# Kernel tuning notes

Measured on AMD Instinct MI355X. Metric: run time of the kernel, lower is better.

The kernel has to match this reference:

```python
import jax, jax.numpy as jnp
import numpy as np

IN_F, OUT_F, GROUP, BITS = 4096, 11008, 128, 4
PACK = 32 // BITS            # 8 nibbles per int32 word
N_GROUPS = IN_F // GROUP     # 32
MASK = (1 << BITS) - 1       # 0xF
TOKENS = 2048


def setup_inputs() -> dict:
    key = jax.random.key(0)
    ks = jax.random.split(key, 6)
    x = jax.random.normal(ks[0], (TOKENS, IN_F), dtype=jnp.float32)
    qweight = jax.random.randint(ks[1], (IN_F // PACK, OUT_F), 0, 2147483647, dtype=jnp.int32)
    qzeros = jax.random.randint(ks[2], (N_GROUPS, OUT_F // PACK), 0, 2147483647, dtype=jnp.int32)
    qscales = jax.random.randint(ks[3], (N_GROUPS, OUT_F), 0, 256, dtype=jnp.int32)  # uint8 values
    qscales_zeros = jax.random.uniform(ks[4], (1, OUT_F), dtype=jnp.float32)
    qscales_scales = jax.random.uniform(ks[5], (1, OUT_F), dtype=jnp.float32) * 0.01
    g_idx = jnp.arange(IN_F, dtype=jnp.int32) // GROUP
    return dict(x=x, qweight=qweight, qzeros=qzeros, qscales=qscales,
                qscales_zeros=qscales_zeros, qscales_scales=qscales_scales, g_idx=g_idx)


def _dequantize(qweight, qzeros, qscales, qscales_zeros, qscales_scales, g_idx, dtype):
    shifts = jnp.arange(0, 32, BITS, dtype=jnp.int32)  # [8]
    # unpack weights: [in/8, 8, out] -> [in, out]
    w = (qweight[:, None, :] >> shifts[None, :, None]) & MASK
    w = w.reshape(-1, qweight.shape[-1])
    # unpack zero-points (+1 per original code): [n_groups, out/8, 8] -> [n_groups, out]
    z = (((qzeros[:, :, None] >> shifts[None, None, :]) & MASK) + 1)
    z = z.reshape(-1, qweight.shape[-1])
    # dequantize the uint8-quantized scales, then apply group-wise
    scales = (qscales.astype(dtype) - qscales_zeros) * qscales_scales  # [n_groups, out]
    return (w - z[g_idx]).astype(dtype) * scales[g_idx]                # [in, out]


def reference(x, qweight, qzeros, qscales, qscales_zeros, qscales_scales, g_idx):
    weight = _dequantize(qweight, qzeros, qscales, qscales_zeros, qscales_scales,
                         g_idx, x.dtype)
    return x @ weight  # bias disabled (disable_bias=True)
```

## Files before the change

kernel.cpp:

```cpp
#include <hip/hip_runtime.h>
#include <hip/hip_fp16.h>
#include <stdint.h>

#define IN_F   4096
#define OUT_F  11008
#define TOKENS 2048
#define BM 128
#define BN 128
#define BK2 128
#define NT2 (IN_F / BK2)
#define NGROUP 32
#define OPW (OUT_F / 8)

typedef _Float16 f16;
typedef __attribute__((ext_vector_type(2))) _Float16 f16x2;
typedef __attribute__((ext_vector_type(8))) _Float16 f16x8;
typedef __attribute__((ext_vector_type(4))) float f32x4;
typedef __attribute__((ext_vector_type(4))) int   i32x4;

typedef __attribute__((address_space(3))) uint32_t lds_u32_t;
typedef const __attribute__((address_space(1))) uint32_t glb_u32_t;

#define SB0() __builtin_amdgcn_sched_barrier(0)

static __device__ __forceinline__ void gload_lds16(const void* g, void* l) {
    __builtin_amdgcn_global_load_lds((glb_u32_t*)g, (lds_u32_t*)l, 16, 0, 0);
}

__global__ __launch_bounds__(256) void quant_x_kernel(const float* __restrict__ x,
                                                      char* __restrict__ xi,
                                                      float* __restrict__ aws) {
    __shared__ float red[4];
    const int row = blockIdx.x;
    const int tid = threadIdx.x;
    const float* xr = x + (size_t)row * IN_F + tid * 16;
    float v[16];
    #pragma unroll
    for (int p = 0; p < 4; ++p) {
        const float4 t = *reinterpret_cast<const float4*>(xr + p * 4);
        v[p * 4 + 0] = t.x; v[p * 4 + 1] = t.y; v[p * 4 + 2] = t.z; v[p * 4 + 3] = t.w;
    }
    float m = 0.f;
    #pragma unroll
    for (int p = 0; p < 16; ++p) m = fmaxf(m, fabsf(v[p]));
    #pragma unroll
    for (int off = 32; off > 0; off >>= 1) m = fmaxf(m, __shfl_xor(m, off));
    if ((tid & 63) == 0) red[tid >> 6] = m;
    __syncthreads();
    m = fmaxf(fmaxf(red[0], red[1]), fmaxf(red[2], red[3]));
    const float a   = m * (1.0f / 127.0f);
    const float inv = (m > 0.f) ? 127.0f / m : 0.f;
    if (tid == 0) aws[row] = a;
    const float MAGIC = 12582912.0f;
    uint32_t b[16];
    #pragma unroll
    for (int p = 0; p < 16; ++p)
        b[p] = __builtin_bit_cast(uint32_t, fmaf(v[p], inv, MAGIC)) & 0xFFu;
    i32x4 d;
    d[0] = (int)(b[0] | (b[2] << 8) | (b[4]  << 16) | (b[6]  << 24));
    d[1] = (int)(b[1] | (b[3] << 8) | (b[5]  << 16) | (b[7]  << 24));
    d[2] = (int)(b[8] | (b[10] << 8) | (b[12] << 16) | (b[14] << 24));
    d[3] = (int)(b[9] | (b[11] << 8) | (b[13] << 16) | (b[15] << 24));
    *reinterpret_cast<i32x4*>(xi + (size_t)row * IN_F + tid * 16) = d;
}

__global__ __launch_bounds__(512, 2) void qgemm_i8_kernel(
    const char*     __restrict__ xi,
    const float*    __restrict__ aws,
    const uint32_t* __restrict__ qweight,
    const uint32_t* __restrict__ qzeros,
    const int*      __restrict__ qscales,
    const float*    __restrict__ qscales_zeros,
    const float*    __restrict__ qscales_scales,
    float*          __restrict__ out)
{
    __shared__ __align__(16) char Ash[2][BM * BK2];
    __shared__ __align__(16) char Bsh[2][BN * BK2];

    const int tid  = threadIdx.x;
    const int lane = tid & 63;
    const int wid  = tid >> 6;
    const int wm   = wid >> 2;
    const int wn   = wid & 3;

    const int mt = blockIdx.x & 15;
    const int nt = blockIdx.x >> 4;
    const int m0 = mt * BM;
    const int n0 = nt * BN;

    const int colb = tid & 127;
    const int h    = tid >> 7;
    const int ncol = n0 + colb;
    const int boff0 = colb * BK2 + ((h)     ^ (colb & 7)) * 16;
    const int boff1 = colb * BK2 + ((h + 4) ^ (colb & 7)) * 16;
    const uint32_t* bptr = qweight + (size_t)(2 * h) * OUT_F + ncol;

    const int arow0 = tid >> 3, aslot0 = tid & 7;
    const int arow1 = (tid + 512) >> 3, aslot1 = (tid + 512) & 7;
    const char* asrc0 = xi + (size_t)(m0 + arow0) * IN_F + (aslot0 ^ (arow0 & 7)) * 16;
    const char* asrc1 = xi + (size_t)(m0 + arow1) * IN_F + (aslot1 ^ (arow1 & 7)) * 16;
    const int adst0 = tid * 16, adst1 = (tid + 512) * 16;

    const int lr = lane & 15;
    const int lo = lane >> 4;
    int aoffr[2][4], boffr[2][2], cread[2];
    #pragma unroll
    for (int ks = 0; ks < 2; ++ks) {
        #pragma unroll
        for (int f = 0; f < 4; ++f) {
            const int ra = wm * 64 + f * 16 + lr;
            aoffr[ks][f] = ra * BK2 + ((ks * 4 + lo) ^ (ra & 7)) * 16;
        }
        #pragma unroll
        for (int j = 0; j < 2; ++j) {
            const int rb = wn * 32 + j * 16 + lr;
            boffr[ks][j] = rb * BK2 + ((ks * 4 + lo) ^ (rb & 7)) * 16;
        }
    }
    cread[0] = n0 + wn * 32 + lr;
    cread[1] = cread[0] + 16;
    float qszr[2], qssr[2];
    #pragma unroll
    for (int j = 0; j < 2; ++j) {
        qszr[j] = qscales_zeros[cread[j]];
        qssr[j] = qscales_scales[cread[j]];
    }

    f32x4 acc[4][2];
    #pragma unroll
    for (int i = 0; i < 4; ++i)
        #pragma unroll
        for (int j = 0; j < 2; ++j) {
            f32x4 z = {0.f, 0.f, 0.f, 0.f};
            acc[i][j] = z;
        }

    auto load_bw = [&](int t_, uint32_t* w) {
        const uint32_t* p = bptr + (size_t)t_ * 16 * OUT_F;
        w[0] = p[0];
        w[1] = p[OUT_F];
        w[2] = p[(size_t)8 * OUT_F];
        w[3] = p[(size_t)9 * OUT_F];
    };
    auto mk_kz = [&](uint32_t zw_) -> uint32_t {
        const uint32_t znib = (zw_ >> ((ncol & 7) * 4)) & 0xFu;
        return (127u - znib) * 0x01010101u;
    };
    auto unpack16 = [&](uint32_t wa, uint32_t wb, uint32_t kz) -> i32x4 {
        i32x4 d;
        d[0] = (int)(((( wa      ) & 0x0F0F0F0Fu) + kz) ^ 0x80808080u);
        d[1] = (int)((((wa >> 4)  & 0x0F0F0F0Fu) + kz) ^ 0x80808080u);
        d[2] = (int)(((( wb      ) & 0x0F0F0F0Fu) + kz) ^ 0x80808080u);
        d[3] = (int)((((wb >> 4)  & 0x0F0F0F0Fu) + kz) ^ 0x80808080u);
        return d;
    };
    auto stage_B = [&](int buf, const uint32_t* w, uint32_t kz) {
        *reinterpret_cast<i32x4*>(&Bsh[buf][boff0]) = unpack16(w[0], w[1], kz);
        *reinterpret_cast<i32x4*>(&Bsh[buf][boff1]) = unpack16(w[2], w[3], kz);
    };
    auto stage_A = [&](int buf, int t_) {
        gload_lds16(asrc0 + (size_t)t_ * BK2, &Ash[buf][adst0]);
        gload_lds16(asrc1 + (size_t)t_ * BK2, &Ash[buf][adst1]);
    };
    auto compute = [&](int buf, const float* sc) {
        i32x4 D[4][2];
        {
            i32x4 af[4], bf[2];
            #pragma unroll
            for (int f = 0; f < 4; ++f)
                af[f] = *reinterpret_cast<const i32x4*>(&Ash[buf][aoffr[0][f]]);
            #pragma unroll
            for (int j = 0; j < 2; ++j)
                bf[j] = *reinterpret_cast<const i32x4*>(&Bsh[buf][boffr[0][j]]);
            __builtin_amdgcn_s_setprio(1);
            #pragma unroll
            for (int i = 0; i < 4; ++i)
                #pragma unroll
                for (int j = 0; j < 2; ++j) {
                    i32x4 z0 = {0, 0, 0, 0};
                    D[i][j] = __builtin_amdgcn_mfma_i32_16x16x64_i8(af[i], bf[j], z0, 0, 0, 0);
                }
            __builtin_amdgcn_s_setprio(0);
        }
        {
            i32x4 af[4], bf[2];
            #pragma unroll
            for (int f = 0; f < 4; ++f)
                af[f] = *reinterpret_cast<const i32x4*>(&Ash[buf][aoffr[1][f]]);
            #pragma unroll
            for (int j = 0; j < 2; ++j)
                bf[j] = *reinterpret_cast<const i32x4*>(&Bsh[buf][boffr[1][j]]);
            __builtin_amdgcn_s_setprio(1);
            #pragma unroll
            for (int i = 0; i < 4; ++i)
                #pragma unroll
                for (int j = 0; j < 2; ++j)
                    D[i][j] = __builtin_amdgcn_mfma_i32_16x16x64_i8(af[i], bf[j], D[i][j], 0, 0, 0);
            __builtin_amdgcn_s_setprio(0);
        }
        #pragma unroll
        for (int i = 0; i < 4; ++i)
            #pragma unroll
            for (int j = 0; j < 2; ++j) {
                acc[i][j].x += sc[j] * (float)D[i][j][0];
                acc[i][j].y += sc[j] * (float)D[i][j][1];
                acc[i][j].z += sc[j] * (float)D[i][j][2];
                acc[i][j].w += sc[j] * (float)D[i][j][3];
            }
    };

    uint32_t wE[4], wO[4];
    uint32_t zwE, zwO;
    int sfE[2], sfO[2];

    {
        uint32_t w0[4];
        load_bw(0, w0);
        const uint32_t kz0 = mk_kz(qzeros[ncol >> 3]);
        stage_A(0, 0);
        stage_B(0, w0, kz0);
        load_bw(1, wE);
        zwE = qzeros[OPW + (ncol >> 3)];
        #pragma unroll
        for (int j = 0; j < 2; ++j) sfE[j] = qscales[cread[j]];
        asm volatile("s_waitcnt vmcnt(0)" ::: "memory");
        asm volatile("s_waitcnt lgkmcnt(0)" ::: "memory");
        __builtin_amdgcn_s_barrier();
    }

#define BODY(C, T, WC, ZC, SFC, WL, ZL, SFL)                                      \
  {                                                                               \
    const int tn1_ = ((T) + 1 < NT2) ? (T) + 1 : NT2 - 1;                         \
    const int tn2_ = ((T) + 2 < NT2) ? (T) + 2 : NT2 - 1;                         \
    float scur_[2];                                                               \
    _Pragma("unroll") for (int j = 0; j < 2; ++j)                                 \
      scur_[j] = ((float)SFC[j] - qszr[j]) * qssr[j];                             \
    const uint32_t kz_ = mk_kz(ZC);                                               \
    stage_B((C) ^ 1, WC, kz_);                                                    \
    SB0();                                                                        \
    stage_A((C) ^ 1, tn1_);                                                       \
    SB0();                                                                        \
    load_bw(tn2_, WL);                                                            \
    ZL = qzeros[(size_t)tn2_ * OPW + (ncol >> 3)];                                \
    _Pragma("unroll") for (int j = 0; j < 2; ++j)                                 \
      SFL[j] = qscales[(size_t)tn1_ * OUT_F + cread[j]];                          \
    SB0();                                                                        \
    compute(C, scur_);                                                            \
    asm volatile("s_waitcnt vmcnt(7)" ::: "memory");                              \
    asm volatile("s_waitcnt lgkmcnt(0)" ::: "memory");                            \
    __builtin_amdgcn_s_barrier();                                                 \
  }

    for (int t = 0; t < NT2; t += 2) {
        BODY(0, t,     wE, zwE, sfE, wO, zwO, sfO)
        BODY(1, t + 1, wO, zwO, sfO, wE, zwE, sfE)
    }
#undef BODY

    const int orow = m0 + wm * 64 + lo * 4;
    const int ocol = n0 + wn * 32 + lr;
    #pragma unroll
    for (int i = 0; i < 4; ++i)
        #pragma unroll
        for (int j = 0; j < 2; ++j)
            #pragma unroll
            for (int r = 0; r < 4; ++r) {
                const int rr = orow + i * 16 + r;
                out[(size_t)rr * OUT_F + ocol + j * 16] = aws[rr] * acc[i][j][r];
            }
}

static __device__ __forceinline__ f16x8 dequant8(uint32_t w, f16x2 sv, f16x2 zv) {
    uint32_t p0 = (w & 0x000F000Fu) | 0x64006400u;
    uint32_t p1 = ((w >> 4)  & 0x000F000Fu) | 0x64006400u;
    uint32_t p2 = ((w >> 8)  & 0x000F000Fu) | 0x64006400u;
    uint32_t p3 = ((w >> 12) & 0x000F000Fu) | 0x64006400u;
    f16x2 h0 = (__builtin_bit_cast(f16x2, p0) + zv) * sv;
    f16x2 h1 = (__builtin_bit_cast(f16x2, p1) + zv) * sv;
    f16x2 h2 = (__builtin_bit_cast(f16x2, p2) + zv) * sv;
    f16x2 h3 = (__builtin_bit_cast(f16x2, p3) + zv) * sv;
    f16x8 o;
    o[0] = h0[0]; o[1] = h0[1]; o[2] = h1[0]; o[3] = h1[1];
    o[4] = h2[0]; o[5] = h2[1]; o[6] = h3[0]; o[7] = h3[1];
    return o;
}

__global__ __launch_bounds__(512, 4) void qgemm_f16_fb(
    const float* __restrict__ x, const uint32_t* __restrict__ qweight,
    const uint32_t* __restrict__ qzeros, const int* __restrict__ qscales,
    const float* __restrict__ qscales_zeros, const float* __restrict__ qscales_scales,
    float* __restrict__ out)
{
    __shared__ __align__(16) f16 heap[2][(BM + BN) * 64];
    f16* const Ab0 = &heap[0][0];
    f16* const Ab1 = &heap[1][0];
    f16* const Bb0 = &heap[0][BM * 64];
    f16* const Bb1 = &heap[1][BM * 64];
    const int tid = threadIdx.x, lane = tid & 63, wid = tid >> 6;
    const int kg = wid >> 2, wm = (wid >> 1) & 1, wn = wid & 1;
    const int mt = blockIdx.x & 15, nt = blockIdx.x >> 4;
    const int m0 = mt * BM, n0 = nt * BN;
    const int colb = tid & 127, og2 = (tid >> 7) << 1, ncol = n0 + colb;
    const float ssv = qscales_scales[ncol], qzssv = qscales_zeros[ncol] * ssv;
    int bo[2];
    #pragma unroll
    for (int r = 0; r < 2; ++r) bo[r] = colb * 64 + ((og2 + r) ^ (colb & 7)) * 8;
    const uint32_t* bptr = qweight + (size_t)og2 * OUT_F + ncol;
    const int arow = tid >> 3, aoct = (tid & 7) ^ (arow & 7);
    const float* fsrc0 = x + (size_t)(m0 + arow) * IN_F + aoct * 8;
    const int aoff0 = tid * 8, aoff1 = (tid + 512) * 8;
    const int lr = lane & 15, lo = lane >> 4, koct = kg * 4 + lo;
    int offA[4], offB[4];
    #pragma unroll
    for (int f = 0; f < 4; ++f) {
        const int ra = wm * 64 + f * 16 + lr;
        offA[f] = ra * 64 + (koct ^ (ra & 7)) * 8;
        const int rb = wn * 64 + f * 16 + lr;
        offB[f] = rb * 64 + (koct ^ (rb & 7)) * 8;
    }
    f32x4 acc[4][4];
    #pragma unroll
    for (int i = 0; i < 4; ++i)
        #pragma unroll
        for (int j = 0; j < 4; ++j) { f32x4 z = {0,0,0,0}; acc[i][j] = z; }
    auto load_bw = [&](int t_, uint32_t* w) {
        const uint32_t* p = bptr + (size_t)t_ * 8 * OUT_F;
        w[0] = p[0]; w[1] = p[OUT_F];
    };
    auto mkc = [&](f16x2& sv_, f16x2& zv_, int sw_, uint32_t zw_) {
        const float sf = (float)sw_ * ssv - qzssv;
        const int z = (int)((zw_ >> ((ncol & 7) * 4)) & 0xFu);
        const f16 sh = (f16)sf, zh = (f16)(float)(-(1025 + z));
        sv_[0] = sh; sv_[1] = sh; zv_[0] = zh; zv_[1] = zh;
    };
    auto stage_B = [&](f16* Bb, const uint32_t* w, f16x2 sv_, f16x2 zv_) {
        *reinterpret_cast<f16x8*>(&Bb[bo[0]]) = dequant8(w[0], sv_, zv_);
        *reinterpret_cast<f16x8*>(&Bb[bo[1]]) = dequant8(w[1], sv_, zv_);
    };
    auto stage_A = [&](f16* Ab, int t_) {
        #pragma unroll
        for (int i = 0; i < 2; ++i) {
            const float* p = fsrc0 + (size_t)t_ * 64 + (size_t)(64 * i) * IN_F;
            const float4 v0 = *reinterpret_cast<const float4*>(p);
            const float4 v1 = *reinterpret_cast<const float4*>(p + 4);
            f16x8 v;
            v[0] = (f16)v0.x; v[1] = (f16)v1.x; v[2] = (f16)v0.y; v[3] = (f16)v1.y;
            v[4] = (f16)v0.z; v[5] = (f16)v1.z; v[6] = (f16)v0.w; v[7] = (f16)v1.w;
            *reinterpret_cast<f16x8*>(&Ab[i == 0 ? aoff0 : aoff1]) = v;
        }
    };
    auto compute = [&](const f16* Ab, const f16* Bb) {
        f16x8 af[4], bf[4];
        #pragma unroll
        for (int f = 0; f < 4; ++f) af[f] = *reinterpret_cast<const f16x8*>(&Ab[offA[f]]);
        #pragma unroll
        for (int f = 0; f < 4; ++f) bf[f] = *reinterpret_cast<const f16x8*>(&Bb[offB[f]]);
        #pragma unroll
        for (int i = 0; i < 4; ++i)
            #pragma unroll
            for (int j = 0; j < 4; ++j)
                acc[i][j] = __builtin_amdgcn_mfma_f32_16x16x32_f16(af[i], bf[j], acc[i][j], 0, 0, 0);
    };
    uint32_t wcur[2], wnxt[2];
    int swN; uint32_t zwN;
    f16x2 sv, zv, svN, zvN;
    {
        uint32_t w0[2];
        load_bw(0, w0);
        const int sw0 = qscales[ncol];
        const uint32_t zw0 = qzeros[ncol >> 3];
        stage_A(Ab0, 0);
        load_bw(1, wcur);
        swN = qscales[OUT_F + ncol]; zwN = qzeros[OPW + (ncol >> 3)];
        mkc(sv, zv, sw0, zw0);
        stage_B(Bb0, w0, sv, zv);
        asm volatile("s_waitcnt lgkmcnt(0)" ::: "memory");
        __builtin_amdgcn_s_barrier();
    }
    for (int t = 0; t < 64; t += 2) {
        mkc(svN, zvN, swN, zwN);
        stage_B(Bb1, wcur, sv, zv);
        stage_A(Ab1, t + 1);
        load_bw(t + 2 < 64 ? t + 2 : 63, wnxt);
        {
            const int g2 = (t >> 1) + 2 < NGROUP ? (t >> 1) + 2 : NGROUP - 1;
            swN = qscales[(size_t)g2 * OUT_F + ncol];
            zwN = qzeros[(size_t)g2 * OPW + (ncol >> 3)];
        }
        compute(Ab0, Bb0);
        asm volatile("s_waitcnt lgkmcnt(0)" ::: "memory");
        __builtin_amdgcn_s_barrier();
        sv = svN; zv = zvN;
        stage_B(Bb0, wnxt, sv, zv);
        stage_A(Ab0, t + 2 < 64 ? t + 2 : 63);
        load_bw(t + 3 < 64 ? t + 3 : 63, wcur);
        compute(Ab1, Bb1);
        asm volatile("s_waitcnt lgkmcnt(0)" ::: "memory");
        __builtin_amdgcn_s_barrier();
    }
    __syncthreads();
    f32x4* scratch = reinterpret_cast<f32x4*>(&heap[0][0]);
    const int wpos = wid & 3;
    #pragma unroll
    for (int hh = 0; hh < 2; ++hh) {
        if (kg == 1) {
            #pragma unroll
            for (int di = 0; di < 2; ++di)
                #pragma unroll
                for (int j = 0; j < 4; ++j)
                    scratch[wpos * 512 + (di * 4 + j) * 64 + lane] = acc[2 * hh + di][j];
        }
        __syncthreads();
        if (kg == 0) {
            #pragma unroll
            for (int di = 0; di < 2; ++di)
                #pragma unroll
                for (int j = 0; j < 4; ++j) {
                    const f32x4 p = scratch[wpos * 512 + (di * 4 + j) * 64 + lane];
                    acc[2 * hh + di][j].x += p.x; acc[2 * hh + di][j].y += p.y;
                    acc[2 * hh + di][j].z += p.z; acc[2 * hh + di][j].w += p.w;
                }
        }
        __syncthreads();
    }
    if (kg == 0) {
        const int orow = m0 + wm * 64 + lo * 4;
        const int ocol = n0 + wn * 64 + lr;
        #pragma unroll
        for (int i = 0; i < 4; ++i)
            #pragma unroll
            for (int j = 0; j < 4; ++j)
                #pragma unroll
                for (int r = 0; r < 4; ++r)
                    out[(size_t)(orow + i * 16 + r) * OUT_F + ocol + j * 16] = acc[i][j][r];
    }
}

extern "C" void kernel_launch(void* const* d_in, const int* in_sizes, int n_in,
                              void* d_out, int out_size, void* d_ws, size_t ws_size,
                              hipStream_t stream) {
    const float*    xp  = (const float*)d_in[0];
    const uint32_t* qw  = (const uint32_t*)d_in[1];
    const uint32_t* qz  = (const uint32_t*)d_in[2];
    const int*      qs  = (const int*)d_in[3];
    const float*    qsz = (const float*)d_in[4];
    const float*    qss = (const float*)d_in[5];
    float* outp = (float*)d_out;

    const int grid = (TOKENS / BM) * (OUT_F / BN);
    const size_t need = (size_t)TOKENS * IN_F + (size_t)TOKENS * 4;

    if (ws_size >= need) {
        char*  xi  = (char*)d_ws;
        float* aws = (float*)(xi + (size_t)TOKENS * IN_F);
        quant_x_kernel<<<TOKENS, 256, 0, stream>>>(xp, xi, aws);
        qgemm_i8_kernel<<<grid, 512, 0, stream>>>(xi, aws, qw, qz, qs, qsz, qss, outp);
    } else {
        qgemm_f16_fb<<<grid, 512, 0, stream>>>(xp, qw, qz, qs, qsz, qss, outp);
    }
}
```

Before: 211.4 us.

## Shrink int8 GEMM tile to 128x64 with BK 64 and 256-thread blocks

Restructures the int8 quantized GEMM to use 128x64 output tiles, a K step of 64 and 256-thread blocks with 4 blocks per CU, instead of 128x128 tiles with K step 128 and 512 threads. Each pair of K steps now covers one quantization group, so the integer MFMA results are carried across two iterations and the group scale is applied only on odd steps. The LDS swizzle, the A/B staging and the zero/scale prefetch indices are reworked to match. The aim is better occupancy and more blocks per wave of the grid. In exchange there are twice as many barriers per group and less data reuse per block, which raises global and LDS traffic.

```diff
diff --git a/kernel.cpp b/kernel.cpp
--- a/kernel.cpp
+++ b/kernel.cpp
@@ -6,9 +6,9 @@
 #define OUT_F  11008
 #define TOKENS 2048
 #define BM 128
-#define BN 128
-#define BK2 128
-#define NT2 (IN_F / BK2)
+#define BN 64
+#define BK 64
+#define NT (IN_F / BK)
 #define NGROUP 32
 #define OPW (OUT_F / 8)
 
@@ -64,7 +64,7 @@
     *reinterpret_cast<i32x4*>(xi + (size_t)row * IN_F + tid * 16) = d;
 }
 
-__global__ __launch_bounds__(512, 2) void qgemm_i8_kernel(
+__global__ __launch_bounds__(256, 4) void qgemm_i8_kernel(
     const char*     __restrict__ xi,
     const float*    __restrict__ aws,
     const uint32_t* __restrict__ qweight,
@@ -74,57 +74,49 @@
     const float*    __restrict__ qscales_scales,
     float*          __restrict__ out)
 {
-    __shared__ __align__(16) char Ash[2][BM * BK2];
-    __shared__ __align__(16) char Bsh[2][BN * BK2];
+    __shared__ __align__(16) char Ash[2][BM * BK];
+    __shared__ __align__(16) char Bsh[2][BN * BK];
 
     const int tid  = threadIdx.x;
     const int lane = tid & 63;
     const int wid  = tid >> 6;
-    const int wm   = wid >> 2;
-    const int wn   = wid & 3;
+    const int wm   = wid >> 1;
+    const int wn   = wid & 1;
 
     const int mt = blockIdx.x & 15;
     const int nt = blockIdx.x >> 4;
     const int m0 = mt * BM;
     const int n0 = nt * BN;
 
-    const int colb = tid & 127;
-    const int h    = tid >> 7;
+    const int colb = tid & 63;
+    const int h    = tid >> 6;
     const int ncol = n0 + colb;
-    const int boff0 = colb * BK2 + ((h)     ^ (colb & 7)) * 16;
-    const int boff1 = colb * BK2 + ((h + 4) ^ (colb & 7)) * 16;
+    const int boff = colb * BK + (h ^ ((colb >> 1) & 3)) * 16;
     const uint32_t* bptr = qweight + (size_t)(2 * h) * OUT_F + ncol;
 
-    const int arow0 = tid >> 3, aslot0 = tid & 7;
-    const int arow1 = (tid + 512) >> 3, aslot1 = (tid + 512) & 7;
-    const char* asrc0 = xi + (size_t)(m0 + arow0) * IN_F + (aslot0 ^ (arow0 & 7)) * 16;
-    const char* asrc1 = xi + (size_t)(m0 + arow1) * IN_F + (aslot1 ^ (arow1 & 7)) * 16;
-    const int adst0 = tid * 16, adst1 = (tid + 512) * 16;
+    const int arow = tid >> 2;
+    const int aunit = (tid & 3) ^ ((arow >> 1) & 3);
+    const char* asrc0 = xi + (size_t)(m0 + arow) * IN_F + aunit * 16;
+    const int adst0 = tid * 16, adst1 = (tid + 256) * 16;
 
     const int lr = lane & 15;
     const int lo = lane >> 4;
-    int aoffr[2][4], boffr[2][2], cread[2];
-    #pragma unroll
-    for (int ks = 0; ks < 2; ++ks) {
-        #pragma unroll
-        for (int f = 0; f < 4; ++f) {
-            const int ra = wm * 64 + f * 16 + lr;
-            aoffr[ks][f] = ra * BK2 + ((ks * 4 + lo) ^ (ra & 7)) * 16;
-        }
-        #pragma unroll
-        for (int j = 0; j < 2; ++j) {
-            const int rb = wn * 32 + j * 16 + lr;
-            boffr[ks][j] = rb * BK2 + ((ks * 4 + lo) ^ (rb & 7)) * 16;
-        }
-    }
-    cread[0] = n0 + wn * 32 + lr;
-    cread[1] = cread[0] + 16;
+    int aoffr[4], boffr[2];
+    #pragma unroll
+    for (int f = 0; f < 4; ++f) {
+        const int ra = wm * 64 + f * 16 + lr;
+        aoffr[f] = ra * BK + ((lo ^ ((ra >> 1) & 3))) * 16;
+    }
+    #pragma unroll
+    for (int j = 0; j < 2; ++j) {
+        const int rb = wn * 32 + j * 16 + lr;
+        boffr[j] = rb * BK + ((lo ^ ((rb >> 1) & 3))) * 16;
+    }
+    const int cread0 = n0 + wn * 32 + lr;
+    const int cread1 = cread0 + 16;
     float qszr[2], qssr[2];
-    #pragma unroll
-    for (int j = 0; j < 2; ++j) {
-        qszr[j] = qscales_zeros[cread[j]];
-        qssr[j] = qscales_scales[cread[j]];
-    }
+    qszr[0] = qscales_zeros[cread0]; qssr[0] = qscales_scales[cread0];
+    qszr[1] = qscales_zeros[cread1]; qssr[1] = qscales_scales[cread1];
 
     f32x4 acc[4][2];
     #pragma unroll
@@ -134,126 +126,105 @@
             f32x4 z = {0.f, 0.f, 0.f, 0.f};
             acc[i][j] = z;
         }
+    i32x4 D[4][2];
 
     auto load_bw = [&](int t_, uint32_t* w) {
-        const uint32_t* p = bptr + (size_t)t_ * 16 * OUT_F;
+        const uint32_t* p = bptr + (size_t)t_ * 8 * OUT_F;
         w[0] = p[0];
         w[1] = p[OUT_F];
-        w[2] = p[(size_t)8 * OUT_F];
-        w[3] = p[(size_t)9 * OUT_F];
     };
     auto mk_kz = [&](uint32_t zw_) -> uint32_t {
         const uint32_t znib = (zw_ >> ((ncol & 7) * 4)) & 0xFu;
         return (127u - znib) * 0x01010101u;
     };
-    auto unpack16 = [&](uint32_t wa, uint32_t wb, uint32_t kz) -> i32x4 {
+    auto stage_B = [&](int buf, const uint32_t* w, uint32_t kz) {
         i32x4 d;
-        d[0] = (int)(((( wa      ) & 0x0F0F0F0Fu) + kz) ^ 0x80808080u);
-        d[1] = (int)((((wa >> 4)  & 0x0F0F0F0Fu) + kz) ^ 0x80808080u);
-        d[2] = (int)(((( wb      ) & 0x0F0F0F0Fu) + kz) ^ 0x80808080u);
-        d[3] = (int)((((wb >> 4)  & 0x0F0F0F0Fu) + kz) ^ 0x80808080u);
-        return d;
-    };
-    auto stage_B = [&](int buf, const uint32_t* w, uint32_t kz) {
-        *reinterpret_cast<i32x4*>(&Bsh[buf][boff0]) = unpack16(w[0], w[1], kz);
-        *reinterpret_cast<i32x4*>(&Bsh[buf][boff1]) = unpack16(w[2], w[3], kz);
+        d[0] = (int)((((w[0]      ) & 0x0F0F0F0Fu) + kz) ^ 0x80808080u);
+        d[1] = (int)((((w[0] >> 4 ) & 0x0F0F0F0Fu) + kz) ^ 0x80808080u);
+        d[2] = (int)((((w[1]      ) & 0x0F0F0F0Fu) + kz) ^ 0x80808080u);
+        d[3] = (int)((((w[1] >> 4 ) & 0x0F0F0F0Fu) + kz) ^ 0x80808080u);
+        *reinterpret_cast<i32x4*>(&Bsh[buf][boff]) = d;
     };
     auto stage_A = [&](int buf, int t_) {
-        gload_lds16(asrc0 + (size_t)t_ * BK2, &Ash[buf][adst0]);
-        gload_lds16(asrc1 + (size_t)t_ * BK2, &Ash[buf][adst1]);
-    };
-    auto compute = [&](int buf, const float* sc) {
-        i32x4 D[4][2];
-        {
-            i32x4 af[4], bf[2];
-            #pragma unroll
-            for (int f = 0; f < 4; ++f)
-                af[f] = *reinterpret_cast<const i32x4*>(&Ash[buf][aoffr[0][f]]);
-            #pragma unroll
-            for (int j = 0; j < 2; ++j)
-                bf[j] = *reinterpret_cast<const i32x4*>(&Bsh[buf][boffr[0][j]]);
-            __builtin_amdgcn_s_setprio(1);
-            #pragma unroll
-            for (int i = 0; i < 4; ++i)
-                #pragma unroll
-                for (int j = 0; j < 2; ++j) {
-                    i32x4 z0 = {0, 0, 0, 0};
-                    D[i][j] = __builtin_amdgcn_mfma_i32_16x16x64_i8(af[i], bf[j], z0, 0, 0, 0);
-                }
-            __builtin_amdgcn_s_setprio(0);
-        }
-        {
-            i32x4 af[4], bf[2];
-            #pragma unroll
-            for (int f = 0; f < 4; ++f)
-                af[f] = *reinterpret_cast<const i32x4*>(&Ash[buf][aoffr[1][f]]);
-            #pragma unroll
-            for (int j = 0; j < 2; ++j)
-                bf[j] = *reinterpret_cast<const i32x4*>(&Bsh[buf][boffr[1][j]]);
-            __builtin_amdgcn_s_setprio(1);
-            #pragma unroll
-            for (int i = 0; i < 4; ++i)
-                #pragma unroll
-                for (int j = 0; j < 2; ++j)
-                    D[i][j] = __builtin_amdgcn_mfma_i32_16x16x64_i8(af[i], bf[j], D[i][j], 0, 0, 0);
-            __builtin_amdgcn_s_setprio(0);
-        }
-        #pragma unroll
-        for (int i = 0; i < 4; ++i)
-            #pragma unroll
-            for (int j = 0; j < 2; ++j) {
-                acc[i][j].x += sc[j] * (float)D[i][j][0];
-                acc[i][j].y += sc[j] * (float)D[i][j][1];
-                acc[i][j].z += sc[j] * (float)D[i][j][2];
-                acc[i][j].w += sc[j] * (float)D[i][j][3];
-            }
-    };
-
-    uint32_t wE[4], wO[4];
+        gload_lds16(asrc0 + (size_t)t_ * BK, &Ash[buf][adst0]);
+        gload_lds16(asrc0 + (size_t)t_ * BK + (size_t)64 * IN_F, &Ash[buf][adst1]);
+    };
+
+    uint32_t wE[2], wO[2];
     uint32_t zwE, zwO;
     int sfE[2], sfO[2];
 
     {
-        uint32_t w0[4];
-        load_bw(0, w0);
-        const uint32_t kz0 = mk_kz(qzeros[ncol >> 3]);
+        uint32_t w00[2];
+        load_bw(0, w00);
+        const uint32_t zw0 = qzeros[ncol >> 3];
         stage_A(0, 0);
-        stage_B(0, w0, kz0);
+        stage_B(0, w00, mk_kz(zw0));
         load_bw(1, wE);
-        zwE = qzeros[OPW + (ncol >> 3)];
-        #pragma unroll
-        for (int j = 0; j < 2; ++j) sfE[j] = qscales[cread[j]];
+        zwE = qzeros[ncol >> 3];
+        sfE[0] = qscales[cread0];
+        sfE[1] = qscales[cread1];
         asm volatile("s_waitcnt vmcnt(0)" ::: "memory");
         asm volatile("s_waitcnt lgkmcnt(0)" ::: "memory");
         __builtin_amdgcn_s_barrier();
     }
 
-#define BODY(C, T, WC, ZC, SFC, WL, ZL, SFL)                                      \
+#define BODY(C, T, WC, ZC, SFC, WL, ZL, SFL, ODD)                                 \
   {                                                                               \
-    const int tn1_ = ((T) + 1 < NT2) ? (T) + 1 : NT2 - 1;                         \
-    const int tn2_ = ((T) + 2 < NT2) ? (T) + 2 : NT2 - 1;                         \
-    float scur_[2];                                                               \
-    _Pragma("unroll") for (int j = 0; j < 2; ++j)                                 \
-      scur_[j] = ((float)SFC[j] - qszr[j]) * qssr[j];                             \
-    const uint32_t kz_ = mk_kz(ZC);                                               \
-    stage_B((C) ^ 1, WC, kz_);                                                    \
-    SB0();                                                                        \
+    const int tn1_ = ((T) + 1 < NT) ? (T) + 1 : NT - 1;                           \
+    const int tn2_ = ((T) + 2 < NT) ? (T) + 2 : NT - 1;                           \
+    const int gz_  = ((T) + 2) >> 1 < NGROUP ? ((T) + 2) >> 1 : NGROUP - 1;       \
+    const int gs_  = ((T) + 1) >> 1 < NGROUP ? ((T) + 1) >> 1 : NGROUP - 1;       \
+    stage_B((C) ^ 1, WC, mk_kz(ZC));                                              \
     stage_A((C) ^ 1, tn1_);                                                       \
     SB0();                                                                        \
     load_bw(tn2_, WL);                                                            \
-    ZL = qzeros[(size_t)tn2_ * OPW + (ncol >> 3)];                                \
-    _Pragma("unroll") for (int j = 0; j < 2; ++j)                                 \
-      SFL[j] = qscales[(size_t)tn1_ * OUT_F + cread[j]];                          \
+    ZL = qzeros[(size_t)gz_ * OPW + (ncol >> 3)];                                 \
+    SFL[0] = qscales[(size_t)gs_ * OUT_F + cread0];                               \
+    SFL[1] = qscales[(size_t)gs_ * OUT_F + cread1];                               \
     SB0();                                                                        \
-    compute(C, scur_);                                                            \
-    asm volatile("s_waitcnt vmcnt(7)" ::: "memory");                              \
+    {                                                                             \
+      i32x4 af[4], bf[2];                                                         \
+      _Pragma("unroll") for (int f = 0; f < 4; ++f)                               \
+        af[f] = *reinterpret_cast<const i32x4*>(&Ash[C][aoffr[f]]);               \
+      _Pragma("unroll") for (int j = 0; j < 2; ++j)                               \
+        bf[j] = *reinterpret_cast<const i32x4*>(&Bsh[C][boffr[j]]);               \
+      __builtin_amdgcn_s_setprio(1);                                              \
+      if (ODD) {                                                                  \
+        _Pragma("unroll") for (int i = 0; i < 4; ++i)                             \
+          _Pragma("unroll") for (int j = 0; j < 2; ++j)                           \
+            D[i][j] = __builtin_amdgcn_mfma_i32_16x16x64_i8(af[i], bf[j],         \
+                                                            D[i][j], 0, 0, 0);   \
+      } else {                                                                    \
+        _Pragma("unroll") for (int i = 0; i < 4; ++i)                             \
+          _Pragma("unroll") for (int j = 0; j < 2; ++j) {                         \
+            i32x4 z0_ = {0, 0, 0, 0};                                             \
+            D[i][j] = __builtin_amdgcn_mfma_i32_16x16x64_i8(af[i], bf[j],         \
+                                                            z0_, 0, 0, 0);       \
+          }                                                                       \
+      }                                                                           \
+      __builtin_amdgcn_s_setprio(0);                                              \
+    }                                                                             \
+    if (ODD) {                                                                    \
+      float scur_[2];                                                             \
+      _Pragma("unroll") for (int j = 0; j < 2; ++j)                               \
+        scur_[j] = ((float)SFC[j] - qszr[j]) * qssr[j];                           \
+      _Pragma("unroll") for (int i = 0; i < 4; ++i)                               \
+        _Pragma("unroll") for (int j = 0; j < 2; ++j) {                           \
+          acc[i][j].x += scur_[j] * (float)D[i][j][0];                            \
+          acc[i][j].y += scur_[j] * (float)D[i][j][1];                            \
+          acc[i][j].z += scur_[j] * (float)D[i][j][2];                            \
+          acc[i][j].w += scur_[j] * (float)D[i][j][3];                            \
+        }                                                                         \
+    }                                                                             \
+    asm volatile("s_waitcnt vmcnt(5)" ::: "memory");                              \
     asm volatile("s_waitcnt lgkmcnt(0)" ::: "memory");                            \
     __builtin_amdgcn_s_barrier();                                                 \
   }
 
-    for (int t = 0; t < NT2; t += 2) {
-        BODY(0, t,     wE, zwE, sfE, wO, zwO, sfO)
-        BODY(1, t + 1, wO, zwO, sfO, wE, zwE, sfE)
+    for (int t = 0; t < NT; t += 2) {
+        BODY(0, t,     wE, zwE, sfE, wO, zwO, sfO, false)
+        BODY(1, t + 1, wO, zwO, sfO, wE, zwE, sfE, true)
     }
 #undef BODY
 
@@ -291,15 +262,15 @@
     const float* __restrict__ qscales_zeros, const float* __restrict__ qscales_scales,
     float* __restrict__ out)
 {
-    __shared__ __align__(16) f16 heap[2][(BM + BN) * 64];
+    __shared__ __align__(16) f16 heap[2][256 * 64];
     f16* const Ab0 = &heap[0][0];
     f16* const Ab1 = &heap[1][0];
-    f16* const Bb0 = &heap[0][BM * 64];
-    f16* const Bb1 = &heap[1][BM * 64];
+    f16* const Bb0 = &heap[0][128 * 64];
+    f16* const Bb1 = &heap[1][128 * 64];
     const int tid = threadIdx.x, lane = tid & 63, wid = tid >> 6;
     const int kg = wid >> 2, wm = (wid >> 1) & 1, wn = wid & 1;
     const int mt = blockIdx.x & 15, nt = blockIdx.x >> 4;
-    const int m0 = mt * BM, n0 = nt * BN;
+    const int m0 = mt * 128, n0 = nt * 128;
     const int colb = tid & 127, og2 = (tid >> 7) << 1, ncol = n0 + colb;
     const float ssv = qscales_scales[ncol], qzssv = qscales_zeros[ncol] * ssv;
     int bo[2];
@@ -447,15 +418,16 @@
     const float*    qss = (const float*)d_in[5];
     float* outp = (float*)d_out;
 
-    const int grid = (TOKENS / BM) * (OUT_F / BN);
     const size_t need = (size_t)TOKENS * IN_F + (size_t)TOKENS * 4;
 
     if (ws_size >= need) {
         char*  xi  = (char*)d_ws;
         float* aws = (float*)(xi + (size_t)TOKENS * IN_F);
         quant_x_kernel<<<TOKENS, 256, 0, stream>>>(xp, xi, aws);
-        qgemm_i8_kernel<<<grid, 512, 0, stream>>>(xi, aws, qw, qz, qs, qsz, qss, outp);
+        const int grid = (TOKENS / BM) * (OUT_F / BN);
+        qgemm_i8_kernel<<<grid, 256, 0, stream>>>(xi, aws, qw, qz, qs, qsz, qss, outp);
     } else {
-        qgemm_f16_fb<<<grid, 512, 0, stream>>>(xp, qw, qz, qs, qsz, qss, outp);
-    }
-}
+        const int gridf = (TOKENS / 128) * (OUT_F / 128);
+        qgemm_f16_fb<<<gridf, 512, 0, stream>>>(xp, qw, qz, qs, qsz, qss, outp);
+    }
+}
```

Result: faster. 179.7 us (-15.0%).
